# Performance work log

Measured on AMD Instinct MI355X. Metric: run time of the kernel, lower is better.

The kernel has to match this reference:

```python
import jax, jax.numpy as jnp
import numpy as np

K = 3
DMAX = 192


def setup_inputs() -> dict:
    key = jax.random.key(0)
    k1, k2 = jax.random.split(key)
    B, C, H, W = 4, 32, 128, 240
    left_img = jax.random.normal(k1, (B, C, H, W), dtype=jnp.float32)
    right_img = jax.random.normal(k2, (B, C, H, W), dtype=jnp.float32)
    return {"left_img": left_img, "right_img": right_img}


def reference(left_img, right_img):
    # D disparity levels at this pyramid scale
    D = DMAX // (2 ** K)
    W = left_img.shape[-1]
    x = jnp.arange(W)[:, None]          # [W, 1]
    d = jnp.arange(D)[None, :]          # [1, D]
    idx = x - d                         # [W, D] source column in right image
    valid = idx >= 0                    # zero-padded region where x < d
    # gather shifted right image: [B, C, H, W, D]
    r_shift = right_img[..., jnp.clip(idx, 0, W - 1)]
    cost = jnp.where(valid, left_img[..., None] - r_shift, jnp.float32(0))
    return cost
```

## Files before the change

kernel.cpp:

```cpp
#include <hip/hip_runtime.h>


constexpr int D_LEVELS = 24;
constexpr int W_IMG = 240;

__global__ __launch_bounds__(256) void cost_volume_kernel(
    const float* __restrict__ left,
    const float* __restrict__ right,
    float4* __restrict__ out,
    int n_pix)
{
    int g = blockIdx.x * blockDim.x + threadIdx.x;
    if (g >= n_pix * 6) return;

    int x_lin = g / 6;
    int j     = g - x_lin * 6;
    int x     = x_lin % W_IMG;
    int row_base = x_lin - x;

    float lv   = left[x_lin];
    int   idx0 = x - 4 * j;

    float4 o;
    {
        int i = idx0 - 0;
        float r = right[row_base + (i > 0 ? i : 0)];
        o.x = (i >= 0) ? (lv - r) : 0.0f;
    }
    {
        int i = idx0 - 1;
        float r = right[row_base + (i > 0 ? i : 0)];
        o.y = (i >= 0) ? (lv - r) : 0.0f;
    }
    {
        int i = idx0 - 2;
        float r = right[row_base + (i > 0 ? i : 0)];
        o.z = (i >= 0) ? (lv - r) : 0.0f;
    }
    {
        int i = idx0 - 3;
        float r = right[row_base + (i > 0 ? i : 0)];
        o.w = (i >= 0) ? (lv - r) : 0.0f;
    }

    out[g] = o;
}

extern "C" void kernel_launch(void* const* d_in, const int* in_sizes, int n_in,
                              void* d_out, int out_size, void* d_ws, size_t ws_size,
                              hipStream_t stream) {
    const float* left  = (const float*)d_in[0];
    const float* right = (const float*)d_in[1];
    float*       out   = (float*)d_out;

    int n_pix = in_sizes[0];
    long long total = (long long)n_pix * 6;
    int  threads = 256;
    int  blocks  = (int)((total + threads - 1) / threads);

    cost_volume_kernel<<<blocks, threads, 0, stream>>>(left, right,
                                                       (float4*)out, n_pix);
}
```

Measured before the change: 436.2 us.

## Stage each image row in shared memory and assign one block per row

Each block now handles one image row. It loads the left and right rows into LDS with float4 loads, and each thread then produces up to six float4 outputs by reading the shifted values from LDS. This replaces the repeated scattered global/L2 gathers of the right image. The kernel is dominated by output writes (about 94 MB), so the gain depends on whether the read side mattered. The change adds a __syncthreads, and some threads sit idle on the last iteration because there are 1440 quads per row against 1536 thread slots.

Result: faster. 389.0 us (-10.8%).

```diff
diff --git a/kernel.cpp b/kernel.cpp
--- a/kernel.cpp
+++ b/kernel.cpp
@@ -1,49 +1,63 @@
 #include <hip/hip_runtime.h>
 
 
-constexpr int D_LEVELS = 24;
 constexpr int W_IMG = 240;
+constexpr int D_LEV = 24;
+constexpr int Q_PER_ROW = W_IMG * D_LEV / 4;
 
 __global__ __launch_bounds__(256) void cost_volume_kernel(
     const float* __restrict__ left,
     const float* __restrict__ right,
-    float4* __restrict__ out,
-    int n_pix)
+    float4* __restrict__ out)
 {
-    int g = blockIdx.x * blockDim.x + threadIdx.x;
-    if (g >= n_pix * 6) return;
+    __shared__ float lrow[W_IMG];
+    __shared__ float rrow[W_IMG];
 
-    int x_lin = g / 6;
-    int j     = g - x_lin * 6;
-    int x     = x_lin % W_IMG;
-    int row_base = x_lin - x;
+    const int row  = blockIdx.x;
+    const int base = row * W_IMG;
+    const int t    = threadIdx.x;
 
-    float lv   = left[x_lin];
-    int   idx0 = x - 4 * j;
+    if (t < 60) {
+        ((float4*)lrow)[t] = ((const float4*)(left + base))[t];
+    } else if (t < 120) {
+        ((float4*)rrow)[t - 60] = ((const float4*)(right + base))[t - 60];
+    }
+    __syncthreads();
 
-    float4 o;
-    {
-        int i = idx0 - 0;
-        float r = right[row_base + (i > 0 ? i : 0)];
-        o.x = (i >= 0) ? (lv - r) : 0.0f;
+    float4* __restrict__ out_row = out + (long long)row * Q_PER_ROW;
+
+    #pragma unroll
+    for (int it = 0; it < 6; ++it) {
+        int q = t + it * 256;
+        if (q < Q_PER_ROW) {
+            int pix = q / 6;
+            int j   = q - pix * 6;
+            int i0  = pix - 4 * j;
+            float lv = lrow[pix];
+            float4 o;
+            {
+                int i = i0 - 0;
+                float r = rrow[i > 0 ? i : 0];
+                o.x = (i >= 0) ? (lv - r) : 0.0f;
+            }
+            {
+                int i = i0 - 1;
+                float r = rrow[i > 0 ? i : 0];
+                o.y = (i >= 0) ? (lv - r) : 0.0f;
+            }
+            {
+                int i = i0 - 2;
+                float r = rrow[i > 0 ? i : 0];
+                o.z = (i >= 0) ? (lv - r) : 0.0f;
+            }
+            {
+                int i = i0 - 3;
+                float r = rrow[i > 0 ? i : 0];
+                o.w = (i >= 0) ? (lv - r) : 0.0f;
+            }
+            out_row[q] = o;
+        }
     }
-    {
-        int i = idx0 - 1;
-        float r = right[row_base + (i > 0 ? i : 0)];
-        o.y = (i >= 0) ? (lv - r) : 0.0f;
-    }
-    {
-        int i = idx0 - 2;
-        float r = right[row_base + (i > 0 ? i : 0)];
-        o.z = (i >= 0) ? (lv - r) : 0.0f;
-    }
-    {
-        int i = idx0 - 3;
-        float r = right[row_base + (i > 0 ? i : 0)];
-        o.w = (i >= 0) ? (lv - r) : 0.0f;
-    }
-
-    out[g] = o;
 }
 
 extern "C" void kernel_launch(void* const* d_in, const int* in_sizes, int n_in,
@@ -54,10 +68,7 @@
     float*       out   = (float*)d_out;
 
     int n_pix = in_sizes[0];
-    long long total = (long long)n_pix * 6;
-    int  threads = 256;
-    int  blocks  = (int)((total + threads - 1) / threads);
+    int rows  = n_pix / W_IMG;
 
-    cost_volume_kernel<<<blocks, threads, 0, stream>>>(left, right,
-                                                       (float4*)out, n_pix);
+    cost_volume_kernel<<<rows, 256, 0, stream>>>(left, right, (float4*)out);
 }
```
